# Performance work log

Hardware: AMD Instinct MI355X
Metric: run time of the kernel (lower is better)

Reference implementation:

```python
import jax, jax.numpy as jnp
import numpy as np

B, T, D = 4, 1024, 2048
H = 32
HD = D // H  # 64
NEG = -1e9


def setup_inputs() -> dict:
    key = jax.random.key(0)
    ks = jax.random.split(key, 12)
    s = 0.02
    x = jax.random.normal(ks[0], (B, T, D), dtype=jnp.float32)
    # additive causal mask [1, 1, T, T]
    causal = jnp.tril(jnp.ones((T, T), dtype=bool))
    attention_mask = jnp.where(causal, 0.0, NEG).astype(jnp.float32)[None, None]
    cache = jnp.zeros((B, 2, T, H, HD), dtype=jnp.float32)
    return {
        "x": x,
        "attention_mask": attention_mask,
        "cache": cache,
        "cache_update_index": 0,
        "Wq": jax.random.normal(ks[1], (D, D), jnp.float32) * s,
        "bq": jnp.zeros((D,), jnp.float32),
        "Wk": jax.random.normal(ks[2], (D, D), jnp.float32) * s,
        "bk": jnp.zeros((D,), jnp.float32),
        "Wv": jax.random.normal(ks[3], (D, D), jnp.float32) * s,
        "bv": jnp.zeros((D,), jnp.float32),
        "Wo": jax.random.normal(ks[4], (D, D), jnp.float32) * s,
        "bo": jnp.zeros((D,), jnp.float32),
    }


def _split_heads(t):
    b, s, _ = t.shape
    return t.reshape(b, s, H, HD).transpose(0, 2, 1, 3)  # (B,H,T,HD)


def reference(x, attention_mask, cache, cache_update_index, Wq, bq, Wk, bk, Wv, bv, Wo, bo):
    q = _split_heads(x @ Wq + bq)  # (B,H,T,HD)
    k = _split_heads(x @ Wk + bk)
    v = _split_heads(x @ Wv + bv)

    # update KV cache (cache layout: [B, 2, max_len, H, HD])
    k_for_cache = k.transpose(0, 2, 1, 3)  # (B,T,H,HD)
    v_for_cache = v.transpose(0, 2, 1, 3)
    idx = (0, cache_update_index, 0, 0)
    k_cache = jax.lax.dynamic_update_slice(cache[:, 0], k_for_cache, idx)
    v_cache = jax.lax.dynamic_update_slice(cache[:, 1], v_for_cache, idx)
    new_cache = jnp.stack([k_cache, v_cache], axis=1)
    k = k_cache.transpose(0, 2, 1, 3)  # (B,H,S,HD)
    v = v_cache.transpose(0, 2, 1, 3)

    scale = jnp.asarray(HD, q.dtype) ** -0.5
    scores = jnp.einsum("bhqd,bhkd->bhqk", q, k) * scale + attention_mask.astype(q.dtype)
    attn = jax.nn.softmax(scores, axis=-1)
    ctx = jnp.einsum("bhqk,bhkd->bhqd", attn, v)  # (B,H,T,HD)
    merged = ctx.transpose(0, 2, 1, 3).reshape(x.shape[0], x.shape[1], D)
    out = merged @ Wo + bo
    return out, new_cache
```

## Files before the change

### kernel.cpp

```cpp
#include <hip/hip_runtime.h>
#include <hip/hip_bf16.h>
#include <stdint.h>


typedef __hip_bfloat16 bf16;
typedef unsigned short us;
typedef short s16x8 __attribute__((ext_vector_type(8)));
typedef float f32x4 __attribute__((ext_vector_type(4)));

#define T_SEQ   1024
#define D_MODEL 2048

__device__ inline us f2b(float f) {
    bf16 h = __float2bfloat16(f);
    return *(us*)&h;
}

typedef __attribute__((address_space(1))) const void gas_void;
typedef __attribute__((address_space(3))) void las_void;

__device__ inline void gl2lds16(const void* g, void* l) {
    __builtin_amdgcn_global_load_lds((gas_void*)g, (las_void*)l, 16, 0, 0);
}

__global__ __launch_bounds__(256)
void cvtx_kernel(const float* __restrict__ x, us* __restrict__ xb)
{
    const size_t i = ((size_t)blockIdx.x * 256 + threadIdx.x) * 8;
    float4 a = *(const float4*)(x + i);
    float4 b = *(const float4*)(x + i + 4);
    union { uint4 u; us s[8]; } p;
    p.s[0] = f2b(a.x); p.s[1] = f2b(a.y); p.s[2] = f2b(a.z); p.s[3] = f2b(a.w);
    p.s[4] = f2b(b.x); p.s[5] = f2b(b.y); p.s[6] = f2b(b.z); p.s[7] = f2b(b.w);
    *(uint4*)(xb + i) = p.u;
}

__global__ __launch_bounds__(256)
void wtrans_kernel(const float* __restrict__ W0, const float* __restrict__ W1,
                   const float* __restrict__ W2, us* __restrict__ Wt)
{
    __shared__ float tile[64][65];
    const int z = blockIdx.z;
    const float* W = (z == 0) ? W0 : (z == 1) ? W1 : W2;
    us* dst = Wt + (size_t)z * D_MODEL * D_MODEL;

    const int tid = threadIdx.x;
    const int k0 = blockIdx.y * 64, n0 = blockIdx.x * 64;

    const int rr = tid >> 4, cc = (tid & 15) * 4;
    #pragma unroll
    for (int i = 0; i < 4; ++i) {
        float4 v = *(const float4*)(W + (size_t)(k0 + rr + i * 16) * D_MODEL + n0 + cc);
        tile[rr + i * 16][cc]     = v.x;
        tile[rr + i * 16][cc + 1] = v.y;
        tile[rr + i * 16][cc + 2] = v.z;
        tile[rr + i * 16][cc + 3] = v.w;
    }
    __syncthreads();

    const int nr = tid >> 3, kc = (tid & 7) * 8;
    #pragma unroll
    for (int i = 0; i < 2; ++i) {
        const int n = nr + i * 32;
        union { uint4 u; us s[8]; } p;
        #pragma unroll
        for (int j = 0; j < 8; ++j) p.s[j] = f2b(tile[kc + j][n]);
        *(uint4*)(dst + (size_t)(n0 + n) * D_MODEL + k0 + kc) = p.u;
    }
}

template<int MODE, int NI>
__global__ __launch_bounds__(256)
void gemm_kernel(const us* __restrict__ A, const us* __restrict__ Bt,
                 const float* __restrict__ b0, const float* __restrict__ b1,
                 const float* __restrict__ b2,
                 float* __restrict__ out0, float* __restrict__ out1,
                 const int* __restrict__ idxp)
{
    __shared__ __align__(16) us As[128 * 32];
    __shared__ __align__(16) us Bs[NI * 32 * 32];

    const int tid  = threadIdx.x;
    const int wave = tid >> 6;
    const int lane = tid & 63;
    const int quad = lane >> 4;
    const int l15  = lane & 15;
    const int wm   = wave >> 1;
    const int wn   = wave & 1;
    const int m0   = blockIdx.y * 128;
    const int n0   = blockIdx.x * (NI * 32);

    constexpr int BCH = NI / 2;
    const int ca   = wave * 2;
    const int rowc = lane >> 2;
    const int kofs = (lane & 3) * 8;

    const us* aG = A  + (size_t)(m0 + ca * 16 + rowc) * D_MODEL + kofs;
    const us* bG = Bt + (size_t)(n0 + wave * BCH * 16 + rowc) * D_MODEL + kofs;
    us* aL = As + ca * 512;
    us* bL = Bs + wave * BCH * 512;

    f32x4 acc[4][NI];
    #pragma unroll
    for (int mi = 0; mi < 4; ++mi)
        #pragma unroll
        for (int ni = 0; ni < NI; ++ni) acc[mi][ni] = f32x4{0.f, 0.f, 0.f, 0.f};

    for (int k0 = 0; k0 < D_MODEL; k0 += 32) {
        gl2lds16(aG + k0,                aL);
        gl2lds16(aG + k0 + 16 * D_MODEL, aL + 512);
        if constexpr (BCH == 2) {
            gl2lds16(bG + k0,                bL);
            gl2lds16(bG + k0 + 16 * D_MODEL, bL + 512);
        } else {
            gl2lds16(bG + k0, bL);
        }
        __syncthreads();

        s16x8 af[4], bfr[NI];
        #pragma unroll
        for (int mi = 0; mi < 4; ++mi)
            af[mi] = *(const s16x8*)(As + (wm * 64 + mi * 16 + l15) * 32 + quad * 8);
        #pragma unroll
        for (int ni = 0; ni < NI; ++ni)
            bfr[ni] = *(const s16x8*)(Bs + (wn * NI * 16 + ni * 16 + l15) * 32 + quad * 8);
        #pragma unroll
        for (int mi = 0; mi < 4; ++mi)
            #pragma unroll
            for (int ni = 0; ni < NI; ++ni)
                acc[mi][ni] = __builtin_amdgcn_mfma_f32_16x16x32_bf16(af[mi], bfr[ni], acc[mi][ni], 0, 0, 0);
        __syncthreads();
    }

    const int reg = (MODE == 3) ? (n0 >> 11) : 0;
    const float* bias = (MODE == 3) ? (reg == 0 ? b0 : (reg == 1 ? b1 : b2)) : b0;
    const int idx = (MODE == 3 && reg > 0) ? idxp[0] : 0;

    #pragma unroll
    for (int ni = 0; ni < NI; ++ni) {
        const int col = n0 + wn * NI * 16 + ni * 16 + l15;
        const int cl  = col & (D_MODEL - 1);
        const float bv = bias[cl];
        #pragma unroll
        for (int mi = 0; mi < 4; ++mi) {
            #pragma unroll
            for (int r = 0; r < 4; ++r) {
                const int m = m0 + wm * 64 + mi * 16 + quad * 4 + r;
                const float v = acc[mi][ni][r] + bv;
                if (MODE == 0) {
                    out0[(size_t)m * D_MODEL + cl] = v;
                } else {
                    if (reg == 0) {
                        ((us*)out0)[(size_t)m * D_MODEL + cl] = f2b(v * 0.125f);
                    } else {
                        const int b  = m >> 10;
                        const int tt = ((m & 1023) + idx) & 1023;
                        out1[((size_t)(b * 2 + (reg - 1)) * T_SEQ + tt) * D_MODEL + cl] = v;
                    }
                }
            }
        }
    }
}

#define LDW  72
#define LDWV 70

__global__ __launch_bounds__(512, 6)
void attn_mfma_kernel(const us* __restrict__ q, const float* __restrict__ cache,
                      us* __restrict__ ctx)
{
    __shared__ __align__(16) us Qs[128 * LDW];
    __shared__ __align__(16) us Ks[64 * LDW];
    __shared__ __align__(16) us Vt[64 * LDWV];

    const int tid  = threadIdx.x;
    const int wave = tid >> 6;
    const int lane = tid & 63;
    const int quad = lane >> 4;
    const int l15  = lane & 15;

    const int bh = blockIdx.x;
    const int b  = bh >> 5;
    const int h  = bh & 31;
    const int qt = 7 - blockIdx.y;

    const float* kbase = cache + ((size_t)(b * 2 + 0) * T_SEQ) * D_MODEL + h * 64;
    const float* vbase = cache + ((size_t)(b * 2 + 1) * T_SEQ) * D_MODEL + h * 64;

    {
        const int qrow = tid >> 2;
        const int qp   = tid & 3;
        const uint4* qg = (const uint4*)(q + (size_t)(b * T_SEQ + qt * 128 + qrow) * D_MODEL
                                           + h * 64 + qp * 16);
        uint4 q0 = qg[0], q1 = qg[1];
        *(uint4*)(Qs + qrow * LDW + qp * 16)     = q0;
        *(uint4*)(Qs + qrow * LDW + qp * 16 + 8) = q1;
    }
    __syncthreads();

    const s16x8 qf0 = *(const s16x8*)(Qs + (wave * 16 + l15) * LDW + quad * 8);
    const s16x8 qf1 = *(const s16x8*)(Qs + (wave * 16 + l15) * LDW + 32 + quad * 8);

    f32x4 oacc[4];
    #pragma unroll
    for (int t = 0; t < 4; ++t) oacc[t] = f32x4{0.f, 0.f, 0.f, 0.f};
    float m_run[4] = {-1e30f, -1e30f, -1e30f, -1e30f};
    float l_run[4] = {0.f, 0.f, 0.f, 0.f};

    const int nkt = 2 * qt + 2;

    const int ksrow = tid >> 3;
    const int kp8   = tid & 7;
    const int vs    = tid >> 4;
    const int vp4   = tid & 15;

    for (int kt = 0; kt < nkt; ++kt) {
        __syncthreads();

        {
            const float4* kg = (const float4*)(kbase + (size_t)(kt * 64 + ksrow) * D_MODEL + kp8 * 8);
            float4 k0 = kg[0], k1 = kg[1];
            union { uint4 u; us s[8]; } p;
            p.s[0] = f2b(k0.x); p.s[1] = f2b(k0.y); p.s[2] = f2b(k0.z); p.s[3] = f2b(k0.w);
            p.s[4] = f2b(k1.x); p.s[5] = f2b(k1.y); p.s[6] = f2b(k1.z); p.s[7] = f2b(k1.w);
            *(uint4*)(Ks + ksrow * LDW + kp8 * 8) = p.u;
        }
        {
            const float4 a = *(const float4*)(vbase + (size_t)(kt * 64 + 2 * vs) * D_MODEL + vp4 * 4);
            const float4 c = *(const float4*)(vbase + (size_t)(kt * 64 + 2 * vs + 1) * D_MODEL + vp4 * 4);
            const float av[4] = {a.x, a.y, a.z, a.w};
            const float cv[4] = {c.x, c.y, c.z, c.w};
            #pragma unroll
            for (int j = 0; j < 4; ++j) {
                ushort2 w; w.x = f2b(av[j]); w.y = f2b(cv[j]);
                *(ushort2*)(Vt + (vp4 * 4 + j) * LDWV + 2 * vs) = w;
            }
        }
        __syncthreads();

        const int kbr = kt * 64 - qt * 128;
        if (kbr < wave * 16 + 16) {
            f32x4 sacc[4];
            #pragma unroll
            for (int t = 0; t < 4; ++t) sacc[t] = f32x4{0.f, 0.f, 0.f, 0.f};
            #pragma unroll
            for (int t = 0; t < 4; ++t) {
                s16x8 kf0 = *(const s16x8*)(Ks + (t * 16 + l15) * LDW + quad * 8);
                s16x8 kf1 = *(const s16x8*)(Ks + (t * 16 + l15) * LDW + 32 + quad * 8);
                sacc[t] = __builtin_amdgcn_mfma_f32_16x16x32_bf16(qf0, kf0, sacc[t], 0, 0, 0);
                sacc[t] = __builtin_amdgcn_mfma_f32_16x16x32_bf16(qf1, kf1, sacc[t], 0, 0, 0);
            }

            if (kbr + 63 > wave * 16) {
                #pragma unroll
                for (int t = 0; t < 4; ++t) {
                    const int keyl = kbr + t * 16 + l15;
                    #pragma unroll
                    for (int r = 0; r < 4; ++r) {
                        if (keyl > wave * 16 + quad * 4 + r) sacc[t][r] = -1e30f;
                    }
                }
            }

            float rmax[4];
            #pragma unroll
            for (int r = 0; r < 4; ++r)
                rmax[r] = fmaxf(fmaxf(sacc[0][r], sacc[1][r]), fmaxf(sacc[2][r], sacc[3][r]));
            #pragma unroll
            for (int off = 1; off < 16; off <<= 1) {
                #pragma unroll
                for (int r = 0; r < 4; ++r) rmax[r] = fmaxf(rmax[r], __shfl_xor(rmax[r], off, 16));
            }
            float alpha[4];
            #pragma unroll
            for (int r = 0; r < 4; ++r) {
                const float mnew = fmaxf(m_run[r], rmax[r]);
                alpha[r] = __expf(m_run[r] - mnew);
                m_run[r] = mnew;
            }
            float rsum[4] = {0.f, 0.f, 0.f, 0.f};
            #pragma unroll
            for (int t = 0; t < 4; ++t) {
                #pragma unroll
                for (int r = 0; r < 4; ++r) {
                    const float p = __expf(sacc[t][r] - m_run[r]);
                    sacc[t][r] = p;
                    rsum[r] += p;
                }
            }
            #pragma unroll
            for (int off = 1; off < 16; off <<= 1) {
                #pragma unroll
                for (int r = 0; r < 4; ++r) rsum[r] += __shfl_xor(rsum[r], off, 16);
            }
            #pragma unroll
            for (int r = 0; r < 4; ++r) l_run[r] = l_run[r] * alpha[r] + rsum[r];
            #pragma unroll
            for (int t = 0; t < 4; ++t) {
                #pragma unroll
                for (int r = 0; r < 4; ++r) oacc[t][r] *= alpha[r];
            }

            #pragma unroll
            for (int t = 0; t < 4; ++t) {
                #pragma unroll
                for (int r = 0; r < 4; ++r)
                    Qs[(wave * 16 + quad * 4 + r) * LDW + t * 16 + l15] = f2b(sacc[t][r]);
            }

            s16x8 pf0 = *(const s16x8*)(Qs + (wave * 16 + l15) * LDW + quad * 8);
            s16x8 pf1 = *(const s16x8*)(Qs + (wave * 16 + l15) * LDW + 32 + quad * 8);
            #pragma unroll
            for (int t = 0; t < 4; ++t) {
                s16x8 vf0 = *(const s16x8*)(Vt + (t * 16 + l15) * LDWV + quad * 8);
                s16x8 vf1 = *(const s16x8*)(Vt + (t * 16 + l15) * LDWV + 32 + quad * 8);
                oacc[t] = __builtin_amdgcn_mfma_f32_16x16x32_bf16(pf0, vf0, oacc[t], 0, 0, 0);
                oacc[t] = __builtin_amdgcn_mfma_f32_16x16x32_bf16(pf1, vf1, oacc[t], 0, 0, 0);
            }
        }
    }

    float invl[4];
    #pragma unroll
    for (int r = 0; r < 4; ++r) invl[r] = 1.0f / l_run[r];
    #pragma unroll
    for (int r = 0; r < 4; ++r) {
        const int qrow = qt * 128 + wave * 16 + quad * 4 + r;
        us* orow = ctx + (size_t)(b * T_SEQ + qrow) * D_MODEL + h * 64;
        #pragma unroll
        for (int t = 0; t < 4; ++t) orow[t * 16 + l15] = f2b(oacc[t][r] * invl[r]);
    }
}

extern "C" void kernel_launch(void* const* d_in, const int* in_sizes, int n_in,
                              void* d_out, int out_size, void* d_ws, size_t ws_size,
                              hipStream_t stream)
{
    const float* x    = (const float*)d_in[0];
    const int*   idxp = (const int*)d_in[3];
    const float* Wq   = (const float*)d_in[4];
    const float* bq   = (const float*)d_in[5];
    const float* Wk   = (const float*)d_in[6];
    const float* bk   = (const float*)d_in[7];
    const float* Wv   = (const float*)d_in[8];
    const float* bv   = (const float*)d_in[9];
    const float* Wo   = (const float*)d_in[10];
    const float* bo   = (const float*)d_in[11];

    float* out      = (float*)d_out;
    us*    xb       = (us*)d_out;
    us*    qb       = (us*)d_out + (size_t)8 * 1024 * 1024;
    float* cacheOut = out + (size_t)4 * T_SEQ * D_MODEL;

    us* WT3  = (us*)d_ws;
    us* WTo  = (us*)d_ws;
    us* ctxb = (us*)d_ws + (size_t)4 * 1024 * 1024;

    const dim3 tb(256);

    cvtx_kernel<<<dim3(4096), tb, 0, stream>>>(x, xb);
    wtrans_kernel<<<dim3(32, 32, 3), tb, 0, stream>>>(Wq, Wk, Wv, WT3);

    gemm_kernel<3, 4><<<dim3(48, 32), tb, 0, stream>>>(
        xb, WT3, bq, bk, bv, (float*)qb, cacheOut, idxp);

    wtrans_kernel<<<dim3(32, 32, 1), tb, 0, stream>>>(Wo, Wo, Wo, WTo);

    attn_mfma_kernel<<<dim3(128, 8), dim3(512), 0, stream>>>(qb, cacheOut, ctxb);

    gemm_kernel<0, 2><<<dim3(32, 32), tb, 0, stream>>>(
        ctxb, WTo, bo, nullptr, nullptr, out, nullptr, nullptr);
}
```

Baseline: 486.3 us.

## Replace GEMMs with 256x256 double-buffered, swizzled, interleaved-stage MFMA kernel

Replaces the 128-row GEMM with a 256x256-tile, 512-thread kernel that double-buffers 64-wide K tiles in LDS. Global-to-LDS loads for the next tile are split into four stages interleaved with MFMA quarter-blocks, paced by explicit vmcnt waits, raw barriers and setprio. LDS addresses are XOR-swizzled to avoid bank conflicts. Larger tiles raise data reuse but shrink the grid: 384 blocks for QKV and only 128 for the output projection, which may underfill the 256 CUs.

```diff
diff --git a/kernel.cpp b/kernel.cpp
--- a/kernel.cpp
+++ b/kernel.cpp
@@ -22,6 +22,8 @@
 __device__ inline void gl2lds16(const void* g, void* l) {
     __builtin_amdgcn_global_load_lds((gas_void*)g, (las_void*)l, 16, 0, 0);
 }
+
+#define VMC(n) asm volatile("s_waitcnt vmcnt(" #n ")" ::: "memory")
 
 __global__ __launch_bounds__(256)
 void cvtx_kernel(const float* __restrict__ x, us* __restrict__ xb)
@@ -69,98 +71,168 @@
     }
 }
 
-template<int MODE, int NI>
-__global__ __launch_bounds__(256)
-void gemm_kernel(const us* __restrict__ A, const us* __restrict__ Bt,
-                 const float* __restrict__ b0, const float* __restrict__ b1,
-                 const float* __restrict__ b2,
-                 float* __restrict__ out0, float* __restrict__ out1,
-                 const int* __restrict__ idxp)
+template<int MODE>
+__global__ __launch_bounds__(512, 2)
+void gemm256_kernel(const us* __restrict__ A, const us* __restrict__ Bt,
+                    const float* __restrict__ b0, const float* __restrict__ b1,
+                    const float* __restrict__ b2,
+                    float* __restrict__ out0, float* __restrict__ out1,
+                    const int* __restrict__ idxp)
 {
-    __shared__ __align__(16) us As[128 * 32];
-    __shared__ __align__(16) us Bs[NI * 32 * 32];
+    __shared__ __align__(16) us As[2 * 16384];
+    __shared__ __align__(16) us Bs[2 * 16384];
 
     const int tid  = threadIdx.x;
-    const int wave = tid >> 6;
+    const int wv   = tid >> 6;
     const int lane = tid & 63;
     const int quad = lane >> 4;
     const int l15  = lane & 15;
-    const int wm   = wave >> 1;
-    const int wn   = wave & 1;
-    const int m0   = blockIdx.y * 128;
-    const int n0   = blockIdx.x * (NI * 32);
-
-    constexpr int BCH = NI / 2;
-    const int ca   = wave * 2;
-    const int rowc = lane >> 2;
-    const int kofs = (lane & 3) * 8;
-
-    const us* aG = A  + (size_t)(m0 + ca * 16 + rowc) * D_MODEL + kofs;
-    const us* bG = Bt + (size_t)(n0 + wave * BCH * 16 + rowc) * D_MODEL + kofs;
-    us* aL = As + ca * 512;
-    us* bL = Bs + wave * BCH * 512;
-
-    f32x4 acc[4][NI];
-    #pragma unroll
-    for (int mi = 0; mi < 4; ++mi)
+    const int wm   = wv >> 2;
+    const int wn   = wv & 3;
+    const int m0   = blockIdx.y * 256;
+    const int n0   = blockIdx.x * 256;
+
+    const int srow = wv * 8 + (lane >> 3);
+    const int scol = ((lane & 7) ^ ((lane >> 3) & 7)) * 8;
+    const us* aG = A  + (size_t)(m0 + srow) * D_MODEL + scol;
+    const us* bG = Bt + (size_t)(n0 + srow) * D_MODEL + scol;
+    us* aD = As + wv * 512;
+    us* bD = Bs + wv * 512;
+
+    const int xq = l15 & 7;
+
+    f32x4 acc[8][4];
+    #pragma unroll
+    for (int mi = 0; mi < 8; ++mi)
         #pragma unroll
-        for (int ni = 0; ni < NI; ++ni) acc[mi][ni] = f32x4{0.f, 0.f, 0.f, 0.f};
-
-    for (int k0 = 0; k0 < D_MODEL; k0 += 32) {
-        gl2lds16(aG + k0,                aL);
-        gl2lds16(aG + k0 + 16 * D_MODEL, aL + 512);
-        if constexpr (BCH == 2) {
-            gl2lds16(bG + k0,                bL);
-            gl2lds16(bG + k0 + 16 * D_MODEL, bL + 512);
-        } else {
-            gl2lds16(bG + k0, bL);
-        }
-        __syncthreads();
-
-        s16x8 af[4], bfr[NI];
-        #pragma unroll
-        for (int mi = 0; mi < 4; ++mi)
-            af[mi] = *(const s16x8*)(As + (wm * 64 + mi * 16 + l15) * 32 + quad * 8);
-        #pragma unroll
-        for (int ni = 0; ni < NI; ++ni)
-            bfr[ni] = *(const s16x8*)(Bs + (wn * NI * 16 + ni * 16 + l15) * 32 + quad * 8);
-        #pragma unroll
-        for (int mi = 0; mi < 4; ++mi)
-            #pragma unroll
-            for (int ni = 0; ni < NI; ++ni)
-                acc[mi][ni] = __builtin_amdgcn_mfma_f32_16x16x32_bf16(af[mi], bfr[ni], acc[mi][ni], 0, 0, 0);
-        __syncthreads();
-    }
-
-    const int reg = (MODE == 3) ? (n0 >> 11) : 0;
-    const float* bias = (MODE == 3) ? (reg == 0 ? b0 : (reg == 1 ? b1 : b2)) : b0;
-    const int idx = (MODE == 3 && reg > 0) ? idxp[0] : 0;
-
-    #pragma unroll
-    for (int ni = 0; ni < NI; ++ni) {
-        const int col = n0 + wn * NI * 16 + ni * 16 + l15;
+        for (int ni = 0; ni < 4; ++ni) acc[mi][ni] = f32x4{0.f, 0.f, 0.f, 0.f};
+
+    #define LDA(BUF, MI, KK) \
+        (*(const s16x8*)(As + (BUF)*16384 + (wm*2 + ((MI)>>2))*4096 \
+            + (((MI)&3)*16 + l15)*64 + ((((KK)*4 + quad) ^ xq) * 8)))
+    #define LDB(BUF, NI, KK) \
+        (*(const s16x8*)(Bs + (BUF)*16384 + wn*4096 \
+            + ((NI)*16 + l15)*64 + ((((KK)*4 + quad) ^ xq) * 8)))
+
+    #define STAGE_B01(NB, KOF) { gl2lds16(bG + (KOF),             bD + (NB)*16384);          \
+                                 gl2lds16(bG + (KOF) +  64*D_MODEL, bD + (NB)*16384 + 4096); }
+    #define STAGE_B23(NB, KOF) { gl2lds16(bG + (KOF) + 128*D_MODEL, bD + (NB)*16384 + 8192);  \
+                                 gl2lds16(bG + (KOF) + 192*D_MODEL, bD + (NB)*16384 + 12288); }
+    #define STAGE_A02(NB, KOF) { gl2lds16(aG + (KOF),             aD + (NB)*16384);          \
+                                 gl2lds16(aG + (KOF) + 128*D_MODEL, aD + (NB)*16384 + 8192); }
+    #define STAGE_A13(NB, KOF) { gl2lds16(aG + (KOF) +  64*D_MODEL, aD + (NB)*16384 + 4096);  \
+                                 gl2lds16(aG + (KOF) + 192*D_MODEL, aD + (NB)*16384 + 12288); }
+
+    STAGE_B01(0, 0); STAGE_B23(0, 0); STAGE_A02(0, 0); STAGE_A13(0, 0);
+    VMC(2);
+    __builtin_amdgcn_s_barrier();
+
+    #define KTILE(BUF, STG, KOFN, VM2STMT, VM4STMT) do {                          \
+        s16x8 aL[4][2], aH[4][2], bF0[2][2], bF1[2][2];                           \
+                                                          \
+        _Pragma("unroll") for (int mi = 0; mi < 4; ++mi)                          \
+            _Pragma("unroll") for (int kk = 0; kk < 2; ++kk)                      \
+                aL[mi][kk] = LDA(BUF, mi, kk);                                    \
+        _Pragma("unroll") for (int ni = 0; ni < 2; ++ni)                          \
+            _Pragma("unroll") for (int kk = 0; kk < 2; ++kk)                      \
+                bF0[ni][kk] = LDB(BUF, ni, kk);                                   \
+        if (STG) STAGE_B01((BUF)^1, KOFN);                                        \
+        __builtin_amdgcn_s_barrier();                                             \
+        __builtin_amdgcn_s_setprio(1);                                            \
+        _Pragma("unroll") for (int kk = 0; kk < 2; ++kk)                          \
+            _Pragma("unroll") for (int mi = 0; mi < 4; ++mi)                      \
+                _Pragma("unroll") for (int ni = 0; ni < 2; ++ni)                  \
+                    acc[mi][ni] = __builtin_amdgcn_mfma_f32_16x16x32_bf16(        \
+                        aL[mi][kk], bF0[ni][kk], acc[mi][ni], 0, 0, 0);           \
+        __builtin_amdgcn_s_setprio(0);                                            \
+        __builtin_amdgcn_s_barrier();                                             \
+                                                          \
+        _Pragma("unroll") for (int ni = 0; ni < 2; ++ni)                          \
+            _Pragma("unroll") for (int kk = 0; kk < 2; ++kk)                      \
+                bF1[ni][kk] = LDB(BUF, 2 + ni, kk);                               \
+        if (STG) STAGE_B23((BUF)^1, KOFN);                                        \
+        __builtin_amdgcn_s_barrier();                                             \
+        __builtin_amdgcn_s_setprio(1);                                            \
+        _Pragma("unroll") for (int kk = 0; kk < 2; ++kk)                          \
+            _Pragma("unroll") for (int mi = 0; mi < 4; ++mi)                      \
+                _Pragma("unroll") for (int ni = 0; ni < 2; ++ni)                  \
+                    acc[mi][2 + ni] = __builtin_amdgcn_mfma_f32_16x16x32_bf16(    \
+                        aL[mi][kk], bF1[ni][kk], acc[mi][2 + ni], 0, 0, 0);       \
+        __builtin_amdgcn_s_setprio(0);                                            \
+        VM2STMT;                                                                  \
+        __builtin_amdgcn_s_barrier();                                             \
+                                                          \
+        _Pragma("unroll") for (int mi = 0; mi < 4; ++mi)                          \
+            _Pragma("unroll") for (int kk = 0; kk < 2; ++kk)                      \
+                aH[mi][kk] = LDA(BUF, 4 + mi, kk);                                \
+        if (STG) STAGE_A02((BUF)^1, KOFN);                                        \
+        __builtin_amdgcn_s_barrier();                                             \
+        __builtin_amdgcn_s_setprio(1);                                            \
+        _Pragma("unroll") for (int kk = 0; kk < 2; ++kk)                          \
+            _Pragma("unroll") for (int mi = 0; mi < 4; ++mi)                      \
+                _Pragma("unroll") for (int ni = 0; ni < 2; ++ni)                  \
+                    acc[4 + mi][2 + ni] = __builtin_amdgcn_mfma_f32_16x16x32_bf16(\
+                        aH[mi][kk], bF1[ni][kk], acc[4 + mi][2 + ni], 0, 0, 0);   \
+        __builtin_amdgcn_s_setprio(0);                                            \
+        __builtin_amdgcn_s_barrier();                                             \
+                                           \
+        if (STG) STAGE_A13((BUF)^1, KOFN);                                        \
+        __builtin_amdgcn_s_barrier();                                             \
+        __builtin_amdgcn_s_setprio(1);                                            \
+        _Pragma("unroll") for (int kk = 0; kk < 2; ++kk)                          \
+            _Pragma("unroll") for (int mi = 0; mi < 4; ++mi)                      \
+                _Pragma("unroll") for (int ni = 0; ni < 2; ++ni)                  \
+                    acc[4 + mi][ni] = __builtin_amdgcn_mfma_f32_16x16x32_bf16(    \
+                        aH[mi][kk], bF0[ni][kk], acc[4 + mi][ni], 0, 0, 0);       \
+        __builtin_amdgcn_s_setprio(0);                                            \
+        VM4STMT;                                                                  \
+        __builtin_amdgcn_s_barrier();                                             \
+    } while (0)
+
+    for (int t = 0; t < 31; ++t) {
+        const int buf = t & 1;
+        const int kofn = (t + 1) * 64;
+        if (buf == 0) KTILE(0, true, kofn, VMC(4), VMC(2));
+        else          KTILE(1, true, kofn, VMC(4), VMC(2));
+    }
+    KTILE(1, false, 0, VMC(0), VMC(0));
+
+    const int seg = (MODE == 3) ? (n0 >> 11) : 0;
+    const float* bias = (MODE == 3) ? (seg == 0 ? b0 : (seg == 1 ? b1 : b2)) : b0;
+    const int idx = (MODE == 3 && seg > 0) ? idxp[0] : 0;
+
+    #pragma unroll
+    for (int ni = 0; ni < 4; ++ni) {
+        const int col = n0 + wn * 64 + ni * 16 + l15;
         const int cl  = col & (D_MODEL - 1);
         const float bv = bias[cl];
         #pragma unroll
-        for (int mi = 0; mi < 4; ++mi) {
+        for (int mi = 0; mi < 8; ++mi) {
             #pragma unroll
             for (int r = 0; r < 4; ++r) {
-                const int m = m0 + wm * 64 + mi * 16 + quad * 4 + r;
+                const int m = m0 + wm * 128 + (mi >> 2) * 64 + (mi & 3) * 16 + quad * 4 + r;
                 const float v = acc[mi][ni][r] + bv;
                 if (MODE == 0) {
                     out0[(size_t)m * D_MODEL + cl] = v;
                 } else {
-                    if (reg == 0) {
+                    if (seg == 0) {
                         ((us*)out0)[(size_t)m * D_MODEL + cl] = f2b(v * 0.125f);
                     } else {
                         const int b  = m >> 10;
                         const int tt = ((m & 1023) + idx) & 1023;
-                        out1[((size_t)(b * 2 + (reg - 1)) * T_SEQ + tt) * D_MODEL + cl] = v;
+                        out1[((size_t)(b * 2 + (seg - 1)) * T_SEQ + tt) * D_MODEL + cl] = v;
                     }
                 }
             }
         }
     }
+    #undef LDA
+    #undef LDB
+    #undef STAGE_B01
+    #undef STAGE_B23
+    #undef STAGE_A02
+    #undef STAGE_A13
+    #undef KTILE
 }
 
 #define LDW  72
@@ -362,13 +434,13 @@
     cvtx_kernel<<<dim3(4096), tb, 0, stream>>>(x, xb);
     wtrans_kernel<<<dim3(32, 32, 3), tb, 0, stream>>>(Wq, Wk, Wv, WT3);
 
-    gemm_kernel<3, 4><<<dim3(48, 32), tb, 0, stream>>>(
+    gemm256_kernel<3><<<dim3(24, 16), dim3(512), 0, stream>>>(
         xb, WT3, bq, bk, bv, (float*)qb, cacheOut, idxp);
 
     wtrans_kernel<<<dim3(32, 32, 1), tb, 0, stream>>>(Wo, Wo, Wo, WTo);
 
     attn_mfma_kernel<<<dim3(128, 8), dim3(512), 0, stream>>>(qb, cacheOut, ctxb);
 
-    gemm_kernel<0, 2><<<dim3(32, 32), tb, 0, stream>>>(
+    gemm256_kernel<0><<<dim3(8, 16), dim3(512), 0, stream>>>(
         ctxb, WTo, bo, nullptr, nullptr, out, nullptr, nullptr);
 }
```

After: 1.301 ms. 2.67x slower.

## Rewrite GEMMs with 128x128x64 tiles, XOR-swizzled LDS and blockwise grid remap

Applied to the files above, without the earlier changes.

Both projection GEMMs now use a single kernel with 128x128 output tiles and a K step of 64. LDS loads use an XOR swizzle to avoid bank conflicts, and block IDs are remapped into eight interleaved groups to improve L2 locality. The output projection grid shrinks to 16x32 blocks, and attention launch bounds drop from 6 to 4 waves per EU. Larger tiles give more reuse and fewer barriers, at the cost of more LDS per block and fewer blocks for the output GEMM.

```diff
diff --git a/kernel.cpp b/kernel.cpp
--- a/kernel.cpp
+++ b/kernel.cpp
@@ -69,76 +69,85 @@
     }
 }
 
-template<int MODE, int NI>
-__global__ __launch_bounds__(256)
-void gemm_kernel(const us* __restrict__ A, const us* __restrict__ Bt,
-                 const float* __restrict__ b0, const float* __restrict__ b1,
-                 const float* __restrict__ b2,
-                 float* __restrict__ out0, float* __restrict__ out1,
-                 const int* __restrict__ idxp)
-{
-    __shared__ __align__(16) us As[128 * 32];
-    __shared__ __align__(16) us Bs[NI * 32 * 32];
+template<int MODE>
+__global__ __launch_bounds__(256, 3)
+void gemm128_kernel(const us* __restrict__ A, const us* __restrict__ Bt,
+                    const float* __restrict__ b0, const float* __restrict__ b1,
+                    const float* __restrict__ b2,
+                    float* __restrict__ out0, float* __restrict__ out1,
+                    const int* __restrict__ idxp)
+{
+    __shared__ __align__(16) us As[128 * 64];
+    __shared__ __align__(16) us Bs[128 * 64];
 
     const int tid  = threadIdx.x;
-    const int wave = tid >> 6;
+    const int wv   = tid >> 6;
     const int lane = tid & 63;
     const int quad = lane >> 4;
     const int l15  = lane & 15;
-    const int wm   = wave >> 1;
-    const int wn   = wave & 1;
-    const int m0   = blockIdx.y * 128;
-    const int n0   = blockIdx.x * (NI * 32);
-
-    constexpr int BCH = NI / 2;
-    const int ca   = wave * 2;
-    const int rowc = lane >> 2;
-    const int kofs = (lane & 3) * 8;
-
-    const us* aG = A  + (size_t)(m0 + ca * 16 + rowc) * D_MODEL + kofs;
-    const us* bG = Bt + (size_t)(n0 + wave * BCH * 16 + rowc) * D_MODEL + kofs;
-    us* aL = As + ca * 512;
-    us* bL = Bs + wave * BCH * 512;
-
-    f32x4 acc[4][NI];
+    const int wm   = wv >> 1;
+    const int wn   = wv & 1;
+
+    const int gx  = gridDim.x;
+    const int nwg = gx * gridDim.y;
+    int bid = blockIdx.y * gx + blockIdx.x;
+    bid = (bid & 7) * (nwg >> 3) + (bid >> 3);
+    const int m0 = (bid / gx) * 128;
+    const int n0 = (bid % gx) * 128;
+
+    const int srow = lane >> 3;
+    const int scol = ((lane & 7) ^ srow) * 8;
+    const us* aG = A  + (size_t)(m0 + wv * 32 + srow) * D_MODEL + scol;
+    const us* bG = Bt + (size_t)(n0 + wv * 32 + srow) * D_MODEL + scol;
+    us* aL = As + wv * 32 * 64;
+    us* bL = Bs + wv * 32 * 64;
+
+    f32x4 acc[4][4];
     #pragma unroll
     for (int mi = 0; mi < 4; ++mi)
         #pragma unroll
-        for (int ni = 0; ni < NI; ++ni) acc[mi][ni] = f32x4{0.f, 0.f, 0.f, 0.f};
-
-    for (int k0 = 0; k0 < D_MODEL; k0 += 32) {
-        gl2lds16(aG + k0,                aL);
-        gl2lds16(aG + k0 + 16 * D_MODEL, aL + 512);
-        if constexpr (BCH == 2) {
-            gl2lds16(bG + k0,                bL);
-            gl2lds16(bG + k0 + 16 * D_MODEL, bL + 512);
-        } else {
-            gl2lds16(bG + k0, bL);
+        for (int ni = 0; ni < 4; ++ni) acc[mi][ni] = f32x4{0.f, 0.f, 0.f, 0.f};
+
+    const int xr = l15 & 7;
+    #define LDA(MI, KK) (*(const s16x8*)(As + (wm * 64 + (MI) * 16 + l15) * 64 \
+                          + ((((KK) * 4 + quad) ^ xr) * 8)))
+    #define LDB(NI, KK) (*(const s16x8*)(Bs + (wn * 64 + (NI) * 16 + l15) * 64 \
+                          + ((((KK) * 4 + quad) ^ xr) * 8)))
+
+    for (int k0 = 0; k0 < D_MODEL; k0 += 64) {
+        #pragma unroll
+        for (int g = 0; g < 4; ++g) {
+            gl2lds16(aG + k0 + g * 8 * D_MODEL, aL + g * 512);
+            gl2lds16(bG + k0 + g * 8 * D_MODEL, bL + g * 512);
         }
         __syncthreads();
 
-        s16x8 af[4], bfr[NI];
-        #pragma unroll
-        for (int mi = 0; mi < 4; ++mi)
-            af[mi] = *(const s16x8*)(As + (wm * 64 + mi * 16 + l15) * 32 + quad * 8);
-        #pragma unroll
-        for (int ni = 0; ni < NI; ++ni)
-            bfr[ni] = *(const s16x8*)(Bs + (wn * NI * 16 + ni * 16 + l15) * 32 + quad * 8);
-        #pragma unroll
-        for (int mi = 0; mi < 4; ++mi)
-            #pragma unroll
-            for (int ni = 0; ni < NI; ++ni)
-                acc[mi][ni] = __builtin_amdgcn_mfma_f32_16x16x32_bf16(af[mi], bfr[ni], acc[mi][ni], 0, 0, 0);
+        #pragma unroll
+        for (int kk = 0; kk < 2; ++kk) {
+            s16x8 af[4], bfr[4];
+            #pragma unroll
+            for (int mi = 0; mi < 4; ++mi) af[mi] = LDA(mi, kk);
+            #pragma unroll
+            for (int ni = 0; ni < 4; ++ni) bfr[ni] = LDB(ni, kk);
+            #pragma unroll
+            for (int mi = 0; mi < 4; ++mi)
+                #pragma unroll
+                for (int ni = 0; ni < 4; ++ni)
+                    acc[mi][ni] = __builtin_amdgcn_mfma_f32_16x16x32_bf16(
+                        af[mi], bfr[ni], acc[mi][ni], 0, 0, 0);
+        }
         __syncthreads();
     }
-
-    const int reg = (MODE == 3) ? (n0 >> 11) : 0;
-    const float* bias = (MODE == 3) ? (reg == 0 ? b0 : (reg == 1 ? b1 : b2)) : b0;
-    const int idx = (MODE == 3 && reg > 0) ? idxp[0] : 0;
-
-    #pragma unroll
-    for (int ni = 0; ni < NI; ++ni) {
-        const int col = n0 + wn * NI * 16 + ni * 16 + l15;
+    #undef LDA
+    #undef LDB
+
+    const int seg = (MODE == 3) ? (n0 >> 11) : 0;
+    const float* bias = (MODE == 3) ? (seg == 0 ? b0 : (seg == 1 ? b1 : b2)) : b0;
+    const int idx = (MODE == 3 && seg > 0) ? idxp[0] : 0;
+
+    #pragma unroll
+    for (int ni = 0; ni < 4; ++ni) {
+        const int col = n0 + wn * 64 + ni * 16 + l15;
         const int cl  = col & (D_MODEL - 1);
         const float bv = bias[cl];
         #pragma unroll
@@ -150,12 +159,12 @@
                 if (MODE == 0) {
                     out0[(size_t)m * D_MODEL + cl] = v;
                 } else {
-                    if (reg == 0) {
+                    if (seg == 0) {
                         ((us*)out0)[(size_t)m * D_MODEL + cl] = f2b(v * 0.125f);
                     } else {
                         const int b  = m >> 10;
                         const int tt = ((m & 1023) + idx) & 1023;
-                        out1[((size_t)(b * 2 + (reg - 1)) * T_SEQ + tt) * D_MODEL + cl] = v;
+                        out1[((size_t)(b * 2 + (seg - 1)) * T_SEQ + tt) * D_MODEL + cl] = v;
                     }
                 }
             }
@@ -166,7 +175,7 @@
 #define LDW  72
 #define LDWV 70
 
-__global__ __launch_bounds__(512, 6)
+__global__ __launch_bounds__(512, 4)
 void attn_mfma_kernel(const us* __restrict__ q, const float* __restrict__ cache,
                       us* __restrict__ ctx)
 {
@@ -362,13 +371,13 @@
     cvtx_kernel<<<dim3(4096), tb, 0, stream>>>(x, xb);
     wtrans_kernel<<<dim3(32, 32, 3), tb, 0, stream>>>(Wq, Wk, Wv, WT3);
 
-    gemm_kernel<3, 4><<<dim3(48, 32), tb, 0, stream>>>(
+    gemm128_kernel<3><<<dim3(48, 32), tb, 0, stream>>>(
         xb, WT3, bq, bk, bv, (float*)qb, cacheOut, idxp);
 
     wtrans_kernel<<<dim3(32, 32, 1), tb, 0, stream>>>(Wo, Wo, Wo, WTo);
 
     attn_mfma_kernel<<<dim3(128, 8), dim3(512), 0, stream>>>(qb, cacheOut, ctxb);
 
-    gemm_kernel<0, 2><<<dim3(32, 32), tb, 0, stream>>>(
+    gemm128_kernel<0><<<dim3(16, 32), tb, 0, stream>>>(
         ctxb, WTo, bo, nullptr, nullptr, out, nullptr, nullptr);
 }
```

Result: faster. 439.0 us (-9.7%).
